# Kernel tuning notes

Measured on AMD Instinct MI355X. Metric: run time of the kernel, lower is better.

## Reference

```python
import jax, jax.numpy as jnp
import numpy as np

B = 262144
N_JOINT = 16
EPS = 1e-12


def skew(w):
    # w: (3,) -> (3,3)
    z = jnp.zeros((), w.dtype)
    return jnp.array([[z, -w[2], w[1]],
                      [w[2], z, -w[0]],
                      [-w[1], w[0], z]])


def srodrigues_batch(tw, q):
    # tw: (6,) screw [w; v], q: (B,) joint values -> (B,4,4) exp([tw]*q)
    w, v = tw[:3], tw[3:]
    theta = jnp.sqrt(jnp.sum(w * w)) + EPS
    wn, vn = w / theta, v / theta
    qt = q * theta                              # (B,)
    W = skew(wn)
    W2 = W @ W
    s = jnp.sin(qt)[:, None, None]
    c = (1.0 - jnp.cos(qt))[:, None, None]
    t = qt[:, None, None]
    I3 = jnp.eye(3, dtype=q.dtype)
    R = I3 + s * W + c * W2                     # (B,3,3)
    G = t * I3 + c * W + (t - s) * W2           # (B,3,3)
    p = jnp.einsum('bij,j->bi', G, vn)          # (B,3)
    top = jnp.concatenate([R, p[..., None]], axis=-1)            # (B,3,4)
    bot = jnp.broadcast_to(jnp.array([0., 0., 0., 1.], q.dtype), (q.shape[0], 1, 4))
    return jnp.concatenate([top, bot], axis=1)


def rpy2r(rpy):
    # ZYX convention: R = Rz(yaw) @ Ry(pitch) @ Rx(roll)
    r, p, y = rpy[0], rpy[1], rpy[2]
    cr, sr = jnp.cos(r), jnp.sin(r)
    cp, sp = jnp.cos(p), jnp.sin(p)
    cy, sy = jnp.cos(y), jnp.sin(y)
    return jnp.array([[cy * cp, cy * sp * sr - sy * cr, cy * sp * cr + sy * sr],
                      [sy * cp, sy * sp * sr + cy * cr, sy * sp * cr - cy * sr],
                      [-sp, cp * sr, cp * cr]])


def pr2t(p, rpy):
    # p: (3,), rpy: (3,) -> (4,4)
    R = rpy2r(rpy)
    top = jnp.concatenate([R, p[:, None]], axis=-1)
    bot = jnp.array([[0., 0., 0., 1.]], R.dtype)
    return jnp.concatenate([top, bot], axis=0)


def poe_forward(q_value, twist, init_p, init_rpy):
    b = q_value.shape[0]
    out0 = jnp.broadcast_to(jnp.eye(4, dtype=q_value.dtype), (b, 4, 4))

    def step(out, xs):
        tw, q = xs                                  # (6,), (B,)
        R = out[:, :3, :3]                          # (B,3,3)
        p = out[:, :3, 3]                           # (B,3)
        w, v = tw[:3], tw[3:]
        # Ad_{T^{-1}} @ tw : [R^T w ; R^T (v - p x w)]
        w_loc = jnp.einsum('bji,j->bi', R, w)
        wb = jnp.broadcast_to(w, (b, 3))
        v_loc = jnp.einsum('bji,bj->bi', R, v - jnp.cross(p, wb))
        tw_local = jnp.concatenate([w_loc, v_loc], axis=-1)   # (B,6)
        out_new = jnp.einsum('bij,bjk->bik', out, srodrigues_batch(tw, q))
        return out_new, tw_local

    out, tw_ls = jax.lax.scan(step, out0, (twist, q_value.T))
    Twistls = jnp.transpose(tw_ls, (1, 0, 2))        # (B, n_joint, 6)
    T_init = pr2t(init_p[0], init_rpy[0])            # (4,4)
    out = jnp.einsum('bij,jk->bik', out, T_init)
    return out, Twistls


def setup_inputs() -> dict:
    key = jax.random.key(0)
    k1, k2, k3, k4 = jax.random.split(key, 4)
    q_value = jax.random.normal(k1, (B, N_JOINT), dtype=jnp.float32)
    twist = jax.random.uniform(k2, (N_JOINT, 6), dtype=jnp.float32, minval=-1.0, maxval=1.0)
    init_p = jax.random.uniform(k3, (1, 3), dtype=jnp.float32, minval=-1.0, maxval=1.0)
    init_rpy = jax.random.uniform(k4, (1, 3), dtype=jnp.float32, minval=-1.0, maxval=1.0)
    return {"q_value": q_value, "twist": twist, "init_p": init_p, "init_rpy": init_rpy}


def reference(q_value, twist, init_p, init_rpy):
    return poe_forward(q_value, twist, init_p, init_rpy)
```

## Files before the change

kernel.cpp:

```cpp
#include <hip/hip_runtime.h>
#include <math.h>

#define NJ  16
#define BLK 256

__global__ __launch_bounds__(BLK) void poe_fwd(
    const float* __restrict__ q,
    const float* __restrict__ twist,
    const float* __restrict__ init_p,
    const float* __restrict__ init_rpy,
    float* __restrict__ outT,
    float* __restrict__ outTw,
    int nb)
{
    int b = blockIdx.x * BLK + threadIdx.x;
    if (b >= nb) return;

    float qv[NJ];
    {
        const float4* q4 = reinterpret_cast<const float4*>(q + (size_t)b * NJ);
        #pragma unroll
        for (int i = 0; i < NJ / 4; ++i) {
            float4 t = q4[i];
            qv[4*i+0] = t.x; qv[4*i+1] = t.y; qv[4*i+2] = t.z; qv[4*i+3] = t.w;
        }
    }

    float R00=1.f, R01=0.f, R02=0.f;
    float R10=0.f, R11=1.f, R12=0.f;
    float R20=0.f, R21=0.f, R22=1.f;
    float p0=0.f, p1=0.f, p2=0.f;

    float hb[48];

    float4* twb4 = reinterpret_cast<float4*>(outTw + (size_t)b * (NJ * 6));

    #pragma unroll
    for (int j = 0; j < NJ; ++j) {
        const float w0 = twist[j*6+0], w1 = twist[j*6+1], w2 = twist[j*6+2];
        const float v0 = twist[j*6+3], v1 = twist[j*6+4], v2 = twist[j*6+5];

        float u0 = v0 - (p1*w2 - p2*w1);
        float u1 = v1 - (p2*w0 - p0*w2);
        float u2 = v2 - (p0*w1 - p1*w0);
        const int o = (j & 7) * 6;
        hb[o+0] = R00*w0 + R10*w1 + R20*w2;
        hb[o+1] = R01*w0 + R11*w1 + R21*w2;
        hb[o+2] = R02*w0 + R12*w1 + R22*w2;
        hb[o+3] = R00*u0 + R10*u1 + R20*u2;
        hb[o+4] = R01*u0 + R11*u1 + R21*u2;
        hb[o+5] = R02*u0 + R12*u1 + R22*u2;

        float ww    = w0*w0 + w1*w1 + w2*w2;
        float theta = sqrtf(ww) + 1e-12f;
        float inv   = 1.0f / theta;
        float wn0 = w0*inv, wn1 = w1*inv, wn2 = w2*inv;
        float vn0 = v0*inv, vn1 = v1*inv, vn2 = v2*inv;
        float qt  = qv[j] * theta;
        float s, cth;
        sincosf(qt, &s, &cth);
        float c  = 1.0f - cth;
        float ts = qt - s;

        float a00 = cth + c*wn0*wn0;
        float a01 = c*wn0*wn1 - s*wn2;
        float a02 = c*wn0*wn2 + s*wn1;
        float a10 = c*wn1*wn0 + s*wn2;
        float a11 = cth + c*wn1*wn1;
        float a12 = c*wn1*wn2 - s*wn0;
        float a20 = c*wn2*wn0 - s*wn1;
        float a21 = c*wn2*wn1 + s*wn0;
        float a22 = cth + c*wn2*wn2;

        float cx0 = wn1*vn2 - wn2*vn1;
        float cx1 = wn2*vn0 - wn0*vn2;
        float cx2 = wn0*vn1 - wn1*vn0;
        float d   = wn0*vn0 + wn1*vn1 + wn2*vn2;
        float td  = ts * d;
        float pj0 = s*vn0 + c*cx0 + td*wn0;
        float pj1 = s*vn1 + c*cx1 + td*wn1;
        float pj2 = s*vn2 + c*cx2 + td*wn2;

        float n00 = R00*a00 + R01*a10 + R02*a20;
        float n01 = R00*a01 + R01*a11 + R02*a21;
        float n02 = R00*a02 + R01*a12 + R02*a22;
        float n10 = R10*a00 + R11*a10 + R12*a20;
        float n11 = R10*a01 + R11*a11 + R12*a21;
        float n12 = R10*a02 + R11*a12 + R12*a22;
        float n20 = R20*a00 + R21*a10 + R22*a20;
        float n21 = R20*a01 + R21*a11 + R22*a21;
        float n22 = R20*a02 + R21*a12 + R22*a22;
        float np0 = R00*pj0 + R01*pj1 + R02*pj2 + p0;
        float np1 = R10*pj0 + R11*pj1 + R12*pj2 + p1;
        float np2 = R20*pj0 + R21*pj1 + R22*pj2 + p2;
        R00=n00; R01=n01; R02=n02;
        R10=n10; R11=n11; R12=n12;
        R20=n20; R21=n21; R22=n22;
        p0=np0; p1=np1; p2=np2;

        if ((j & 7) == 7) {
            const int base = (j >> 3) * 12;
            #pragma unroll
            for (int k = 0; k < 12; ++k)
                twb4[base + k] =
                    make_float4(hb[4*k+0], hb[4*k+1], hb[4*k+2], hb[4*k+3]);
        }
    }

    float rr = init_rpy[0], pt = init_rpy[1], yw = init_rpy[2];
    float sr, cr, sp, cp, sy, cy;
    sincosf(rr, &sr, &cr);
    sincosf(pt, &sp, &cp);
    sincosf(yw, &sy, &cy);
    float i00 = cy*cp, i01 = cy*sp*sr - sy*cr, i02 = cy*sp*cr + sy*sr;
    float i10 = sy*cp, i11 = sy*sp*sr + cy*cr, i12 = sy*sp*cr - cy*sr;
    float i20 = -sp,   i21 = cp*sr,            i22 = cp*cr;
    float ip0 = init_p[0], ip1 = init_p[1], ip2 = init_p[2];

    float f00 = R00*i00 + R01*i10 + R02*i20;
    float f01 = R00*i01 + R01*i11 + R02*i21;
    float f02 = R00*i02 + R01*i12 + R02*i22;
    float f10 = R10*i00 + R11*i10 + R12*i20;
    float f11 = R10*i01 + R11*i11 + R12*i21;
    float f12 = R10*i02 + R11*i12 + R12*i22;
    float f20 = R20*i00 + R21*i10 + R22*i20;
    float f21 = R20*i01 + R21*i11 + R22*i21;
    float f22 = R20*i02 + R21*i12 + R22*i22;
    float fp0 = R00*ip0 + R01*ip1 + R02*ip2 + p0;
    float fp1 = R10*ip0 + R11*ip1 + R12*ip2 + p1;
    float fp2 = R20*ip0 + R21*ip1 + R22*ip2 + p2;

    float4* o4 = reinterpret_cast<float4*>(outT + (size_t)b * 16);
    o4[0] = make_float4(f00, f01, f02, fp0);
    o4[1] = make_float4(f10, f11, f12, fp1);
    o4[2] = make_float4(f20, f21, f22, fp2);
    o4[3] = make_float4(0.f, 0.f, 0.f, 1.f);
}

extern "C" void kernel_launch(void* const* d_in, const int* in_sizes, int n_in,
                              void* d_out, int out_size, void* d_ws, size_t ws_size,
                              hipStream_t stream) {
    const float* q        = (const float*)d_in[0];
    const float* twist    = (const float*)d_in[1];
    const float* init_p   = (const float*)d_in[2];
    const float* init_rpy = (const float*)d_in[3];

    int nb = in_sizes[0] / NJ;
    float* outT  = (float*)d_out;
    float* outTw = outT + (size_t)nb * 16;

    int blocks = (nb + BLK - 1) / BLK;
    poe_fwd<<<blocks, BLK, 0, stream>>>(q, twist, init_p, init_rpy, outT, outTw, nb);
}
```

Measured before the change: 50.00 us.

## Stage twist and transform outputs through LDS for coalesced wave-wide stores

Each wave writes its per-thread twist halves and final transforms into a padded LDS buffer, then reads them back in a transposed order so that consecutive lanes store consecutive float4s to global memory. The goal is to replace strided per-thread 16-byte stores with fully coalesced ones. It adds LDS traffic, about 53 KB of shared memory per block that may limit occupancy, and integer divides for indexing. The bounds check and partial-block handling are removed, so the kernel assumes the batch is a multiple of 256.

Result: no change. 49.44 us (-1.1%).

```diff
diff --git a/kernel.cpp b/kernel.cpp
--- a/kernel.cpp
+++ b/kernel.cpp
@@ -1,8 +1,9 @@
 #include <hip/hip_runtime.h>
 #include <math.h>
 
-#define NJ  16
-#define BLK 256
+#define NJ    16
+#define BLK   256
+#define WAVES (BLK / 64)
 
 __global__ __launch_bounds__(BLK) void poe_fwd(
     const float* __restrict__ q,
@@ -13,8 +14,14 @@
     float* __restrict__ outTw,
     int nb)
 {
-    int b = blockIdx.x * BLK + threadIdx.x;
-    if (b >= nb) return;
+    __shared__ float4 lds4[WAVES * 64 * 13];
+
+    const int tid  = threadIdx.x;
+    const int lane = tid & 63;
+    const int wid  = tid >> 6;
+    float4* wbuf = &lds4[wid * (64 * 13)];
+
+    const int b = blockIdx.x * BLK + tid;
 
     float qv[NJ];
     {
@@ -33,7 +40,8 @@
 
     float hb[48];
 
-    float4* twb4 = reinterpret_cast<float4*>(outTw + (size_t)b * (NJ * 6));
+    float4* twdst = reinterpret_cast<float4*>(outTw) +
+                    (size_t)(blockIdx.x * BLK + wid * 64) * 24;
 
     #pragma unroll
     for (int j = 0; j < NJ; ++j) {
@@ -99,11 +107,18 @@
         p0=np0; p1=np1; p2=np2;
 
         if ((j & 7) == 7) {
-            const int base = (j >> 3) * 12;
             #pragma unroll
             for (int k = 0; k < 12; ++k)
-                twb4[base + k] =
+                wbuf[lane * 13 + k] =
                     make_float4(hb[4*k+0], hb[4*k+1], hb[4*k+2], hb[4*k+3]);
+            const int h = j >> 3;
+            #pragma unroll
+            for (int i = 0; i < 12; ++i) {
+                int g  = i * 64 + lane;
+                int r  = g / 12;
+                int k4 = g - r * 12;
+                twdst[r * 24 + h * 12 + k4] = wbuf[r * 13 + k4];
+            }
         }
     }
 
@@ -130,11 +145,19 @@
     float fp1 = R10*ip0 + R11*ip1 + R12*ip2 + p1;
     float fp2 = R20*ip0 + R21*ip1 + R22*ip2 + p2;
 
-    float4* o4 = reinterpret_cast<float4*>(outT + (size_t)b * 16);
-    o4[0] = make_float4(f00, f01, f02, fp0);
-    o4[1] = make_float4(f10, f11, f12, fp1);
-    o4[2] = make_float4(f20, f21, f22, fp2);
-    o4[3] = make_float4(0.f, 0.f, 0.f, 1.f);
+    wbuf[lane * 13 + 0] = make_float4(f00, f01, f02, fp0);
+    wbuf[lane * 13 + 1] = make_float4(f10, f11, f12, fp1);
+    wbuf[lane * 13 + 2] = make_float4(f20, f21, f22, fp2);
+    wbuf[lane * 13 + 3] = make_float4(0.f, 0.f, 0.f, 1.f);
+    float4* tdst = reinterpret_cast<float4*>(outT) +
+                   (size_t)(blockIdx.x * BLK + wid * 64) * 4;
+    #pragma unroll
+    for (int i = 0; i < 4; ++i) {
+        int g  = i * 64 + lane;
+        int r  = g >> 2;
+        int k4 = g & 3;
+        tdst[g] = wbuf[r * 13 + k4];
+    }
 }
 
 extern "C" void kernel_launch(void* const* d_in, const int* in_sizes, int n_in,
@@ -149,6 +172,6 @@
     float* outT  = (float*)d_out;
     float* outTw = outT + (size_t)nb * 16;
 
-    int blocks = (nb + BLK - 1) / BLK;
+    int blocks = nb / BLK;
     poe_fwd<<<blocks, BLK, 0, stream>>>(q, twist, init_p, init_rpy, outT, outTw, nb);
 }
```

## Split each batch element across four lanes with shuffle-based parallel prefix of transforms

Applied to the files above, without the earlier changes.

Each batch element is now handled by four threads, each owning four joints. The threads build local products of their joint transforms and combine them with a warp-shuffle Hillis-Steele prefix scan to get each segment's starting pose. Each thread then writes its four local twists as float2 stores and one row of the final pose. The aim is more parallelism and coalesced stores. The cost is extra matrix products, recomputation of buildA, 12-wide shuffles, and fast __sinf/__cosf intrinsics that may lose accuracy for large arguments.

Result: faster. 47.42 us (-5.2%).

```diff
diff --git a/kernel.cpp b/kernel.cpp
--- a/kernel.cpp
+++ b/kernel.cpp
@@ -3,6 +3,48 @@
 
 #define NJ  16
 #define BLK 256
+
+struct Mat { float m[12]; };
+
+__device__ __forceinline__ Mat mul(const Mat& A, const Mat& B) {
+    Mat C;
+    #pragma unroll
+    for (int r = 0; r < 3; ++r) {
+        float a0 = A.m[3*r+0], a1 = A.m[3*r+1], a2 = A.m[3*r+2];
+        C.m[3*r+0] = a0*B.m[0] + a1*B.m[3] + a2*B.m[6];
+        C.m[3*r+1] = a0*B.m[1] + a1*B.m[4] + a2*B.m[7];
+        C.m[3*r+2] = a0*B.m[2] + a1*B.m[5] + a2*B.m[8];
+        C.m[9+r]   = a0*B.m[9] + a1*B.m[10] + a2*B.m[11] + A.m[9+r];
+    }
+    return C;
+}
+
+__device__ __forceinline__ Mat buildA(const float* tw6, float qj) {
+    float w0 = tw6[0], w1 = tw6[1], w2 = tw6[2];
+    float v0 = tw6[3], v1 = tw6[4], v2 = tw6[5];
+    float theta = sqrtf(w0*w0 + w1*w1 + w2*w2) + 1e-12f;
+    float inv   = __builtin_amdgcn_rcpf(theta);
+    float wn0 = w0*inv, wn1 = w1*inv, wn2 = w2*inv;
+    float vn0 = v0*inv, vn1 = v1*inv, vn2 = v2*inv;
+    float qt  = qj * theta;
+    float s   = __sinf(qt);
+    float cth = __cosf(qt);
+    float c   = 1.0f - cth;
+    float ts  = qt - s;
+    Mat A;
+    A.m[0] = cth + c*wn0*wn0;  A.m[1] = c*wn0*wn1 - s*wn2; A.m[2] = c*wn0*wn2 + s*wn1;
+    A.m[3] = c*wn1*wn0 + s*wn2; A.m[4] = cth + c*wn1*wn1;  A.m[5] = c*wn1*wn2 - s*wn0;
+    A.m[6] = c*wn2*wn0 - s*wn1; A.m[7] = c*wn2*wn1 + s*wn0; A.m[8] = cth + c*wn2*wn2;
+    float cx0 = wn1*vn2 - wn2*vn1;
+    float cx1 = wn2*vn0 - wn0*vn2;
+    float cx2 = wn0*vn1 - wn1*vn0;
+    float d   = wn0*vn0 + wn1*vn1 + wn2*vn2;
+    float td  = ts * d;
+    A.m[9]  = s*vn0 + c*cx0 + td*wn0;
+    A.m[10] = s*vn1 + c*cx1 + td*wn1;
+    A.m[11] = s*vn2 + c*cx2 + td*wn2;
+    return A;
+}
 
 __global__ __launch_bounds__(BLK) void poe_fwd(
     const float* __restrict__ q,
@@ -13,128 +55,105 @@
     float* __restrict__ outTw,
     int nb)
 {
-    int b = blockIdx.x * BLK + threadIdx.x;
-    if (b >= nb) return;
+    const int g    = blockIdx.x * BLK + threadIdx.x;
+    const int e    = g >> 2;
+    const int s    = g & 3;
+    const int lane = threadIdx.x & 63;
+    if (e >= nb) return;
 
-    float qv[NJ];
+    float qk[4];
     {
-        const float4* q4 = reinterpret_cast<const float4*>(q + (size_t)b * NJ);
+        float4 t = reinterpret_cast<const float4*>(q)[(size_t)e * 4 + s];
+        qk[0] = t.x; qk[1] = t.y; qk[2] = t.z; qk[3] = t.w;
+    }
+
+    float tws[24];
+    {
+        const float4* t4 = reinterpret_cast<const float4*>(twist) + s * 6;
         #pragma unroll
-        for (int i = 0; i < NJ / 4; ++i) {
-            float4 t = q4[i];
-            qv[4*i+0] = t.x; qv[4*i+1] = t.y; qv[4*i+2] = t.z; qv[4*i+3] = t.w;
+        for (int i = 0; i < 6; ++i) {
+            float4 t = t4[i];
+            tws[4*i+0] = t.x; tws[4*i+1] = t.y; tws[4*i+2] = t.z; tws[4*i+3] = t.w;
         }
     }
 
-    float R00=1.f, R01=0.f, R02=0.f;
-    float R10=0.f, R11=1.f, R12=0.f;
-    float R20=0.f, R21=0.f, R22=1.f;
-    float p0=0.f, p1=0.f, p2=0.f;
-
-    float hb[48];
-
-    float4* twb4 = reinterpret_cast<float4*>(outTw + (size_t)b * (NJ * 6));
+    Mat P = buildA(&tws[0], qk[0]);
+    #pragma unroll
+    for (int k = 1; k < 4; ++k)
+        P = mul(P, buildA(&tws[6*k], qk[k]));
 
     #pragma unroll
-    for (int j = 0; j < NJ; ++j) {
-        const float w0 = twist[j*6+0], w1 = twist[j*6+1], w2 = twist[j*6+2];
-        const float v0 = twist[j*6+3], v1 = twist[j*6+4], v2 = twist[j*6+5];
+    for (int step = 1; step < 4; step <<= 1) {
+        const bool use = (s >= step);
+        const int  src = use ? lane - step : lane;
+        Mat T;
+        #pragma unroll
+        for (int i = 0; i < 12; ++i) T.m[i] = __shfl(P.m[i], src, 64);
+        Mat M = mul(T, P);
+        #pragma unroll
+        for (int i = 0; i < 12; ++i) P.m[i] = use ? M.m[i] : P.m[i];
+    }
 
+    Mat pose;
+    {
+        const int src = (s == 0) ? lane : lane - 1;
+        #pragma unroll
+        for (int i = 0; i < 12; ++i) pose.m[i] = __shfl(P.m[i], src, 64);
+        const float id[12] = {1,0,0, 0,1,0, 0,0,1, 0,0,0};
+        #pragma unroll
+        for (int i = 0; i < 12; ++i) pose.m[i] = (s == 0) ? id[i] : pose.m[i];
+    }
+
+    float2* twb = reinterpret_cast<float2*>(outTw) + (size_t)g * 12;
+    #pragma unroll
+    for (int k = 0; k < 4; ++k) {
+        const float* t6 = &tws[6*k];
+        float w0 = t6[0], w1 = t6[1], w2 = t6[2];
+        float v0 = t6[3], v1 = t6[4], v2 = t6[5];
+        float p0 = pose.m[9], p1 = pose.m[10], p2 = pose.m[11];
         float u0 = v0 - (p1*w2 - p2*w1);
         float u1 = v1 - (p2*w0 - p0*w2);
         float u2 = v2 - (p0*w1 - p1*w0);
-        const int o = (j & 7) * 6;
-        hb[o+0] = R00*w0 + R10*w1 + R20*w2;
-        hb[o+1] = R01*w0 + R11*w1 + R21*w2;
-        hb[o+2] = R02*w0 + R12*w1 + R22*w2;
-        hb[o+3] = R00*u0 + R10*u1 + R20*u2;
-        hb[o+4] = R01*u0 + R11*u1 + R21*u2;
-        hb[o+5] = R02*u0 + R12*u1 + R22*u2;
-
-        float ww    = w0*w0 + w1*w1 + w2*w2;
-        float theta = sqrtf(ww) + 1e-12f;
-        float inv   = 1.0f / theta;
-        float wn0 = w0*inv, wn1 = w1*inv, wn2 = w2*inv;
-        float vn0 = v0*inv, vn1 = v1*inv, vn2 = v2*inv;
-        float qt  = qv[j] * theta;
-        float s, cth;
-        sincosf(qt, &s, &cth);
-        float c  = 1.0f - cth;
-        float ts = qt - s;
-
-        float a00 = cth + c*wn0*wn0;
-        float a01 = c*wn0*wn1 - s*wn2;
-        float a02 = c*wn0*wn2 + s*wn1;
-        float a10 = c*wn1*wn0 + s*wn2;
-        float a11 = cth + c*wn1*wn1;
-        float a12 = c*wn1*wn2 - s*wn0;
-        float a20 = c*wn2*wn0 - s*wn1;
-        float a21 = c*wn2*wn1 + s*wn0;
-        float a22 = cth + c*wn2*wn2;
-
-        float cx0 = wn1*vn2 - wn2*vn1;
-        float cx1 = wn2*vn0 - wn0*vn2;
-        float cx2 = wn0*vn1 - wn1*vn0;
-        float d   = wn0*vn0 + wn1*vn1 + wn2*vn2;
-        float td  = ts * d;
-        float pj0 = s*vn0 + c*cx0 + td*wn0;
-        float pj1 = s*vn1 + c*cx1 + td*wn1;
-        float pj2 = s*vn2 + c*cx2 + td*wn2;
-
-        float n00 = R00*a00 + R01*a10 + R02*a20;
-        float n01 = R00*a01 + R01*a11 + R02*a21;
-        float n02 = R00*a02 + R01*a12 + R02*a22;
-        float n10 = R10*a00 + R11*a10 + R12*a20;
-        float n11 = R10*a01 + R11*a11 + R12*a21;
-        float n12 = R10*a02 + R11*a12 + R12*a22;
-        float n20 = R20*a00 + R21*a10 + R22*a20;
-        float n21 = R20*a01 + R21*a11 + R22*a21;
-        float n22 = R20*a02 + R21*a12 + R22*a22;
-        float np0 = R00*pj0 + R01*pj1 + R02*pj2 + p0;
-        float np1 = R10*pj0 + R11*pj1 + R12*pj2 + p1;
-        float np2 = R20*pj0 + R21*pj1 + R22*pj2 + p2;
-        R00=n00; R01=n01; R02=n02;
-        R10=n10; R11=n11; R12=n12;
-        R20=n20; R21=n21; R22=n22;
-        p0=np0; p1=np1; p2=np2;
-
-        if ((j & 7) == 7) {
-            const int base = (j >> 3) * 12;
-            #pragma unroll
-            for (int k = 0; k < 12; ++k)
-                twb4[base + k] =
-                    make_float4(hb[4*k+0], hb[4*k+1], hb[4*k+2], hb[4*k+3]);
-        }
+        float wl0 = pose.m[0]*w0 + pose.m[3]*w1 + pose.m[6]*w2;
+        float wl1 = pose.m[1]*w0 + pose.m[4]*w1 + pose.m[7]*w2;
+        float wl2 = pose.m[2]*w0 + pose.m[5]*w1 + pose.m[8]*w2;
+        float vl0 = pose.m[0]*u0 + pose.m[3]*u1 + pose.m[6]*u2;
+        float vl1 = pose.m[1]*u0 + pose.m[4]*u1 + pose.m[7]*u2;
+        float vl2 = pose.m[2]*u0 + pose.m[5]*u1 + pose.m[8]*u2;
+        twb[3*k+0] = make_float2(wl0, wl1);
+        twb[3*k+1] = make_float2(wl2, vl0);
+        twb[3*k+2] = make_float2(vl1, vl2);
+        if (k < 3)
+            pose = mul(pose, buildA(t6, qk[k]));
     }
 
+    Mat F;
+    {
+        const int src = lane | 3;
+        #pragma unroll
+        for (int i = 0; i < 12; ++i) F.m[i] = __shfl(P.m[i], src, 64);
+    }
     float rr = init_rpy[0], pt = init_rpy[1], yw = init_rpy[2];
-    float sr, cr, sp, cp, sy, cy;
-    sincosf(rr, &sr, &cr);
-    sincosf(pt, &sp, &cp);
-    sincosf(yw, &sy, &cy);
+    float sr = __sinf(rr), cr = __cosf(rr);
+    float sp = __sinf(pt), cp = __cosf(pt);
+    float sy = __sinf(yw), cy = __cosf(yw);
     float i00 = cy*cp, i01 = cy*sp*sr - sy*cr, i02 = cy*sp*cr + sy*sr;
     float i10 = sy*cp, i11 = sy*sp*sr + cy*cr, i12 = sy*sp*cr - cy*sr;
     float i20 = -sp,   i21 = cp*sr,            i22 = cp*cr;
     float ip0 = init_p[0], ip1 = init_p[1], ip2 = init_p[2];
 
-    float f00 = R00*i00 + R01*i10 + R02*i20;
-    float f01 = R00*i01 + R01*i11 + R02*i21;
-    float f02 = R00*i02 + R01*i12 + R02*i22;
-    float f10 = R10*i00 + R11*i10 + R12*i20;
-    float f11 = R10*i01 + R11*i11 + R12*i21;
-    float f12 = R10*i02 + R11*i12 + R12*i22;
-    float f20 = R20*i00 + R21*i10 + R22*i20;
-    float f21 = R20*i01 + R21*i11 + R22*i21;
-    float f22 = R20*i02 + R21*i12 + R22*i22;
-    float fp0 = R00*ip0 + R01*ip1 + R02*ip2 + p0;
-    float fp1 = R10*ip0 + R11*ip1 + R12*ip2 + p1;
-    float fp2 = R20*ip0 + R21*ip1 + R22*ip2 + p2;
+    float r0 = (s == 0) ? F.m[0] : (s == 1) ? F.m[3] : F.m[6];
+    float r1 = (s == 0) ? F.m[1] : (s == 1) ? F.m[4] : F.m[7];
+    float r2 = (s == 0) ? F.m[2] : (s == 1) ? F.m[5] : F.m[8];
+    float pr = (s == 0) ? F.m[9] : (s == 1) ? F.m[10] : F.m[11];
+    float4 row;
+    row.x = r0*i00 + r1*i10 + r2*i20;
+    row.y = r0*i01 + r1*i11 + r2*i21;
+    row.z = r0*i02 + r1*i12 + r2*i22;
+    row.w = r0*ip0 + r1*ip1 + r2*ip2 + pr;
+    if (s == 3) row = make_float4(0.f, 0.f, 0.f, 1.f);
 
-    float4* o4 = reinterpret_cast<float4*>(outT + (size_t)b * 16);
-    o4[0] = make_float4(f00, f01, f02, fp0);
-    o4[1] = make_float4(f10, f11, f12, fp1);
-    o4[2] = make_float4(f20, f21, f22, fp2);
-    o4[3] = make_float4(0.f, 0.f, 0.f, 1.f);
+    reinterpret_cast<float4*>(outT)[(size_t)g] = row;
 }
 
 extern "C" void kernel_launch(void* const* d_in, const int* in_sizes, int n_in,
@@ -149,6 +168,7 @@
     float* outT  = (float*)d_out;
     float* outTw = outT + (size_t)nb * 16;
 
-    int blocks = (nb + BLK - 1) / BLK;
+    int threads = nb * 4;
+    int blocks  = (threads + BLK - 1) / BLK;
     poe_fwd<<<blocks, BLK, 0, stream>>>(q, twist, init_p, init_rpy, outT, outTw, nb);
 }
```
